# Kernel tuning notes

Hardware: AMD Instinct MI355X
Metric: run time of the kernel (lower is better)

## Reference

```python
import jax, jax.numpy as jnp
import numpy as np

NEG_SLOPE = 0.05

def setup_inputs() -> dict:
    key = jax.random.key(0)
    k1, k2, k3, k4 = jax.random.split(key, 4)
    N, C, n, l = 100000, 128, 50000, 32
    z = jax.random.normal(k1, (N, C), dtype=jnp.float32)
    # indices into table of N+1 rows (row 0 is the zero_holder pad row)
    neighbor = jax.random.randint(k2, (n, l), 0, N + 1, dtype=jnp.int64)
    w1 = jax.random.normal(k3, (C // 2, C), dtype=jnp.float32) * (1.0 / np.sqrt(C))
    w2 = jax.random.normal(k4, (C - C // 2, C // 2), dtype=jnp.float32) * (1.0 / np.sqrt(C // 2))
    return {"z": z, "neighbor": neighbor, "w1": w1, "w2": w2}

def reference(z, neighbor, w1, w2):
    # prepend zero_holder row; z is detached in the original module
    z_ = jnp.concatenate([jnp.zeros((1, z.shape[1]), dtype=z.dtype), z], axis=0)
    z_ = jax.lax.stop_gradient(z_)
    x = z_[neighbor]                       # [n, l, C] embedding gather
    # conv1d(kernel_size=1, bias=False) == per-position linear
    h1 = jnp.einsum('nlc,oc->nlo', x, w1)  # [n, l, C/2]
    h1 = jnp.where(h1 > 0, h1, NEG_SLOPE * h1)
    # dropout is identity in eval mode
    h2 = jnp.einsum('nlc,oc->nlo', h1, w2)  # [n, l, C - C/2]
    h2 = jnp.where(h2 > 0, h2, NEG_SLOPE * h2)
    cat = jnp.concatenate([h1, h2], axis=-1)  # [n, l, C]
    return jnp.max(cat, axis=1)               # adaptive_max_pool1d over l -> [n, C]
```

## Files before the change

### kernel.cpp

```cpp
#include <hip/hip_runtime.h>
#include <hip/hip_bf16.h>

typedef __attribute__((ext_vector_type(8))) short bf16x8;
typedef __attribute__((ext_vector_type(4))) short s16x4;
typedef __attribute__((ext_vector_type(4))) float f32x4;

__device__ __forceinline__ short f2bf(float f) {
    __hip_bfloat16 h = __float2bfloat16(f);
    short s;
    __builtin_memcpy(&s, &h, 2);
    return s;
}

__device__ __forceinline__ float bf2f(short s) {
    const unsigned u = (unsigned)(unsigned short)s;
    return __uint_as_float(u << 16);
}

__device__ __forceinline__ float lrelu(float v) {
    return fmaxf(v, 0.05f * v);
}

#define MFMA(a, b, c) __builtin_amdgcn_mfma_f32_16x16x32_bf16((a), (b), (c), 0, 0, 0)

__global__ __launch_bounds__(256) void mlp_rows_q8_kernel(
    const float* __restrict__ z,
    const float* __restrict__ w1,
    const float* __restrict__ w2,
    char* __restrict__ q8,
    float* __restrict__ scales,
    int rows_p1)
{
    __shared__ __align__(16) short wlds[12288];

    const int tid = threadIdx.x;
    const int lane = tid & 63;
    const int g = lane >> 4;
    const int u = lane & 15;

    #pragma unroll
    for (int j = 0; j < 12; ++j) {
        const int c = tid + (j << 8);
        const float* src;
        int row, col, fbase;
        if (c < 2048) {
            row = c >> 5; col = (c & 31) << 2;
            src = w1 + row * 128 + col;
            fbase = ((row >> 4) << 2) + (col >> 5);
        } else {
            const int c2 = c - 2048;
            row = c2 >> 4; col = (c2 & 15) << 2;
            src = w2 + row * 64 + col;
            fbase = 16 + ((row >> 4) << 1) + (col >> 5);
        }
        const int rem = col & 31;
        const int gg = (rem >> 2) & 3;
        const int eh = rem >> 4;
        float4 v = *reinterpret_cast<const float4*>(src);
        s16x4 p;
        p[0] = f2bf(v.x); p[1] = f2bf(v.y); p[2] = f2bf(v.z); p[3] = f2bf(v.w);
        const int idx = ((fbase << 6) + (gg << 4) + (row & 15)) * 8 + (eh << 2);
        *reinterpret_cast<s16x4*>(&wlds[idx]) = p;
    }
    __syncthreads();

    const bf16x8* __restrict__ wv = reinterpret_cast<const bf16x8*>(wlds);

    const int waves_per_blk = blockDim.x >> 6;
    const int wave = blockIdx.x * waves_per_blk + (tid >> 6);
    const int nwaves = gridDim.x * waves_per_blk;
    const int ntiles = (rows_p1 + 15) >> 4;

    for (int c = wave; c < ntiles; c += nwaves) {
        const int r = (c << 4) + u;
        const bool valid = (r >= 1) && (r < rows_p1);
        const bool st = r < rows_p1;

        bf16x8 bx[4];
        {
            const float* srcp = z + (size_t)(r - 1) * 128 + 4 * g;
            #pragma unroll
            for (int s = 0; s < 4; ++s) {
                float4 lo = make_float4(0.f, 0.f, 0.f, 0.f);
                float4 hi = make_float4(0.f, 0.f, 0.f, 0.f);
                if (valid) {
                    lo = *reinterpret_cast<const float4*>(srcp + 32 * s);
                    hi = *reinterpret_cast<const float4*>(srcp + 32 * s + 16);
                }
                bf16x8 f;
                f[0] = f2bf(lo.x); f[1] = f2bf(lo.y); f[2] = f2bf(lo.z); f[3] = f2bf(lo.w);
                f[4] = f2bf(hi.x); f[5] = f2bf(hi.y); f[6] = f2bf(hi.z); f[7] = f2bf(hi.w);
                bx[s] = f;
            }
        }

        char* qp = q8 + (size_t)r * 128 + 4 * g;

        f32x4 d2[4];
        #pragma unroll
        for (int b2 = 0; b2 < 4; ++b2)
            d2[b2] = (f32x4){0.f, 0.f, 0.f, 0.f};

        bf16x8 h1sav[2];

        #pragma unroll
        for (int s2 = 0; s2 < 2; ++s2) {
            bf16x8 p2;
            #pragma unroll
            for (int h = 0; h < 2; ++h) {
                const int b = 2 * s2 + h;
                f32x4 d1 = (f32x4){0.f, 0.f, 0.f, 0.f};
                #pragma unroll
                for (int s = 0; s < 4; ++s)
                    d1 = MFMA(wv[((b << 2) + s) * 64 + lane], bx[s], d1);
                #pragma unroll
                for (int q = 0; q < 4; ++q)
                    p2[4 * h + q] = f2bf(lrelu(d1[q]));
            }
            h1sav[s2] = p2;
            #pragma unroll
            for (int b2 = 0; b2 < 4; ++b2)
                d2[b2] = MFMA(wv[1024 + ((b2 << 1) + s2) * 64 + lane], p2, d2[b2]);
        }

        {
            float s1 = 0.f;
            #pragma unroll
            for (int s2 = 0; s2 < 2; ++s2)
                #pragma unroll
                for (int i = 0; i < 8; ++i)
                    s1 = fmaxf(s1, fabsf(bf2f(h1sav[s2][i])));
            s1 = fmaxf(s1, __shfl_xor(s1, 16, 64));
            s1 = fmaxf(s1, __shfl_xor(s1, 32, 64));
            const float inv = (s1 > 0.f) ? 127.f / s1 : 0.f;
            if (g == 0 && st) scales[2 * r + 0] = s1 * (1.f / 127.f);
            #pragma unroll
            for (int b = 0; b < 4; ++b) {
                unsigned pk = 0;
                #pragma unroll
                for (int q = 0; q < 4; ++q) {
                    const float hv = bf2f(h1sav[b >> 1][4 * (b & 1) + q]);
                    const int qi = __float2int_rn(hv * inv);
                    pk |= ((unsigned)(qi & 0xff)) << (8 * q);
                }
                if (st) *reinterpret_cast<unsigned*>(qp + 16 * b) = pk;
            }
        }

        {
            float s2m = 0.f;
            #pragma unroll
            for (int b2 = 0; b2 < 4; ++b2)
                #pragma unroll
                for (int q = 0; q < 4; ++q)
                    s2m = fmaxf(s2m, fabsf(lrelu(d2[b2][q])));
            s2m = fmaxf(s2m, __shfl_xor(s2m, 16, 64));
            s2m = fmaxf(s2m, __shfl_xor(s2m, 32, 64));
            const float inv = (s2m > 0.f) ? 127.f / s2m : 0.f;
            if (g == 0 && st) scales[2 * r + 1] = s2m * (1.f / 127.f);
            #pragma unroll
            for (int b2 = 0; b2 < 4; ++b2) {
                unsigned pk = 0;
                #pragma unroll
                for (int q = 0; q < 4; ++q) {
                    const int qi = __float2int_rn(lrelu(d2[b2][q]) * inv);
                    pk |= ((unsigned)(qi & 0xff)) << (8 * q);
                }
                if (st) *reinterpret_cast<unsigned*>(qp + 64 + 16 * b2) = pk;
            }
        }
    }
}

__global__ __launch_bounds__(256) void gather_max_q8_kernel(
    const char* __restrict__ q8,
    const float* __restrict__ scales,
    const int* __restrict__ neigh,
    float* __restrict__ out,
    int n_rows)
{
    const int tid = threadIdx.x;
    const int lane = tid & 63;
    const int hsel = lane >> 5;
    const int waves_per_blk = blockDim.x >> 6;
    const int wave0 = blockIdx.x * waves_per_blk + (tid >> 6);
    const int nwaves = gridDim.x * waves_per_blk;

    for (int n = wave0; n < n_rows; n += nwaves) {
        const int idxv = neigh[(size_t)n * 32 + (lane & 31)];
        const float sv = scales[(size_t)2 * (unsigned)idxv + hsel];

        unsigned short d[32];
        #pragma unroll
        for (int p = 0; p < 32; ++p) {
            const unsigned rp = (unsigned)__builtin_amdgcn_readlane(idxv, p);
            d[p] = *reinterpret_cast<const unsigned short*>(
                q8 + (size_t)rp * 128 + 2 * lane);
        }

        float m0 = -3.4e38f, m1 = -3.4e38f;
        #pragma unroll
        for (int p = 0; p < 32; ++p) {
            const float sc = __shfl(sv, (lane & 32) + p, 64);
            const int q0 = (int)(signed char)(d[p] & 0xff);
            const int q1 = (int)(signed char)(d[p] >> 8);
            m0 = fmaxf(m0, (float)q0 * sc);
            m1 = fmaxf(m1, (float)q1 * sc);
        }

        *reinterpret_cast<float2*>(out + (size_t)n * 128 + 2 * lane) =
            make_float2(m0, m1);
    }
}

struct WaveCtx {
    const bf16x8* wv;
    const int* neigh;
    float* out;
    int lane, g, u, n_rows;
};

__device__ __forceinline__ void compute_n(const WaveCtx& cx, bf16x8 (&bx)[2][4], int n)
{
    f32x4 d2[4][2];
    #pragma unroll
    for (int b2 = 0; b2 < 4; ++b2) {
        d2[b2][0] = (f32x4){0.f, 0.f, 0.f, 0.f};
        d2[b2][1] = (f32x4){0.f, 0.f, 0.f, 0.f};
    }
    float V1[16], V2[16];

    #pragma unroll
    for (int s2 = 0; s2 < 2; ++s2) {
        bf16x8 p2[2];
        #pragma unroll
        for (int h = 0; h < 2; ++h) {
            const int b = 2 * s2 + h;
            f32x4 d1[2];
            d1[0] = (f32x4){0.f, 0.f, 0.f, 0.f};
            d1[1] = (f32x4){0.f, 0.f, 0.f, 0.f};
            #pragma unroll
            for (int s = 0; s < 4; ++s) {
                const bf16x8 wf = cx.wv[((b << 2) + s) * 64 + cx.lane];
                d1[0] = MFMA(wf, bx[0][s], d1[0]);
                d1[1] = MFMA(wf, bx[1][s], d1[1]);
            }
            #pragma unroll
            for (int t = 0; t < 2; ++t) {
                #pragma unroll
                for (int q = 0; q < 4; ++q) {
                    float v = lrelu(d1[t][q]);
                    d1[t][q] = v;
                    p2[t][4 * h + q] = f2bf(v);
                }
            }
            #pragma unroll
            for (int q = 0; q < 4; ++q)
                V1[b * 4 + q] = fmaxf(d1[0][q], d1[1][q]);
        }
        #pragma unroll
        for (int b2 = 0; b2 < 4; ++b2) {
            const bf16x8 wf = cx.wv[1024 + ((b2 << 1) + s2) * 64 + cx.lane];
            d2[b2][0] = MFMA(wf, p2[0], d2[b2][0]);
            d2[b2][1] = MFMA(wf, p2[1], d2[b2][1]);
        }
    }

    #pragma unroll
    for (int b2 = 0; b2 < 4; ++b2) {
        #pragma unroll
        for (int q = 0; q < 4; ++q)
            V2[b2 * 4 + q] = lrelu(fmaxf(d2[b2][0][q], d2[b2][1][q]));
    }

    const int u = cx.u;
    #pragma unroll
    for (int k = 0; k < 4; ++k) {
        const int m = 1 << k;
        const bool hi = (u & m) != 0;
        #pragma unroll
        for (int j = 0; j < (8 >> k); ++j) {
            float k1 = hi ? V1[2 * j + 1] : V1[2 * j];
            float s1 = hi ? V1[2 * j] : V1[2 * j + 1];
            float k2 = hi ? V2[2 * j + 1] : V2[2 * j];
            float s2v = hi ? V2[2 * j] : V2[2 * j + 1];
            V1[j] = fmaxf(k1, __shfl_xor(s1, m, 64));
            V2[j] = fmaxf(k2, __shfl_xor(s2v, m, 64));
        }
    }

    const int l = cx.lane;
    const int src = 16 * ((l >> 2) & 3) + ((l >> 4) << 2) + (l & 3);
    float v1 = __shfl(V1[0], src, 64);
    float v2 = __shfl(V2[0], src, 64);
    float* op = cx.out + (size_t)n * 128;
    op[l] = v1;
    op[64 + l] = v2;
}

__global__ __launch_bounds__(256, 3) void neigh_enco_fp32_kernel(
    const float* __restrict__ z,
    const int* __restrict__ neigh,
    const float* __restrict__ w1,
    const float* __restrict__ w2,
    float* __restrict__ out,
    int n_rows, int z_rows)
{
    __shared__ __align__(16) short wlds[12288];
    const int tid = threadIdx.x;
    const int lane = tid & 63;
    const int g = lane >> 4;
    const int u = lane & 15;

    #pragma unroll
    for (int j = 0; j < 12; ++j) {
        const int c = tid + (j << 8);
        const float* src;
        int row, col, fbase;
        if (c < 2048) {
            row = c >> 5; col = (c & 31) << 2;
            src = w1 + row * 128 + col;
            fbase = ((row >> 4) << 2) + (col >> 5);
        } else {
            const int c2 = c - 2048;
            row = c2 >> 4; col = (c2 & 15) << 2;
            src = w2 + row * 64 + col;
            fbase = 16 + ((row >> 4) << 1) + (col >> 5);
        }
        const int rem = col & 31;
        const int gg = (rem >> 2) & 3;
        const int eh = rem >> 4;
        float4 v = *reinterpret_cast<const float4*>(src);
        s16x4 p;
        p[0] = f2bf(v.x); p[1] = f2bf(v.y); p[2] = f2bf(v.z); p[3] = f2bf(v.w);
        const int idx = ((fbase << 6) + (gg << 4) + (row & 15)) * 8 + (eh << 2);
        *reinterpret_cast<s16x4*>(&wlds[idx]) = p;
    }
    __syncthreads();

    WaveCtx cx;
    cx.wv = reinterpret_cast<const bf16x8*>(wlds);
    cx.neigh = neigh; cx.out = out;
    cx.lane = lane; cx.g = g; cx.u = u; cx.n_rows = n_rows;

    const int waves_per_blk = blockDim.x >> 6;
    const int wave = blockIdx.x * waves_per_blk + (tid >> 6);
    const int nwaves = gridDim.x * waves_per_blk;
    const unsigned zu = (unsigned)z_rows;

    for (int n = wave; n < n_rows; n += nwaves) {
        unsigned r0 = (unsigned)neigh[n * 32 + u] - 1u;
        unsigned r1 = (unsigned)neigh[n * 32 + 16 + u] - 1u;
        bf16x8 bx[2][4];
        #pragma unroll
        for (int t = 0; t < 2; ++t) {
            const unsigned r = t ? r1 : r0;
            const bool valid = r < zu;
            const float* base = z + (size_t)r * 128 + 4 * g;
            #pragma unroll
            for (int s = 0; s < 4; ++s) {
                float4 lo = make_float4(0.f, 0.f, 0.f, 0.f);
                float4 hi = make_float4(0.f, 0.f, 0.f, 0.f);
                if (valid) {
                    lo = *reinterpret_cast<const float4*>(base + 32 * s);
                    hi = *reinterpret_cast<const float4*>(base + 32 * s + 16);
                }
                bf16x8 f;
                f[0] = f2bf(lo.x); f[1] = f2bf(lo.y); f[2] = f2bf(lo.z); f[3] = f2bf(lo.w);
                f[4] = f2bf(hi.x); f[5] = f2bf(hi.y); f[6] = f2bf(hi.z); f[7] = f2bf(hi.w);
                bx[t][s] = f;
            }
        }
        compute_n(cx, bx, n);
    }
}

extern "C" void kernel_launch(void* const* d_in, const int* in_sizes, int n_in,
                              void* d_out, int out_size, void* d_ws, size_t ws_size,
                              hipStream_t stream) {
    const float* z     = (const float*)d_in[0];
    const int*   neigh = (const int*)d_in[1];
    const float* w1    = (const float*)d_in[2];
    const float* w2    = (const float*)d_in[3];
    float* out = (float*)d_out;
    const int z_rows = in_sizes[0] / 128;
    const int n_rows = in_sizes[1] / 32;
    const int rows_p1 = z_rows + 1;

    const size_t q8_bytes = (size_t)rows_p1 * 128;
    const size_t need = q8_bytes + (size_t)rows_p1 * 2 * sizeof(float);
    if (ws_size >= need) {
        char* q8 = (char*)d_ws;
        float* scales = (float*)((char*)d_ws + q8_bytes);
        const int ntiles = (rows_p1 + 15) / 16;
        const int blocks = (ntiles + 3) / 4;
        hipLaunchKernelGGL(mlp_rows_q8_kernel, dim3(blocks), dim3(256),
                           0, stream, z, w1, w2, q8, scales, rows_p1);
        hipLaunchKernelGGL(gather_max_q8_kernel, dim3(2048), dim3(256), 0, stream,
                           q8, scales, neigh, out, n_rows);
    } else {
        hipLaunchKernelGGL(neigh_enco_fp32_kernel, dim3(2048), dim3(256), 0, stream,
                           z, neigh, w1, w2, out, n_rows, z_rows);
    }
}
```

Baseline: 59.17 us.

## Stage z tiles through swizzled LDS and load gather scales per neighbor

The MLP kernel now cooperatively loads a 64-row chunk of z into LDS with coalesced float4 reads, converting to bf16 once and XOR-swizzling to avoid bank conflicts. Each wave then reads its MFMA operands from LDS instead of issuing strided global loads. The gather kernel drops the cross-lane shuffle for scales and instead loads both scales per neighbor row as a float2, processing neighbors in two halves of 16 to lower register pressure, and its grid is doubled. The per-chunk syncs add barrier overhead, and the extra LDS lowers occupancy in the MLP kernel.

After: 64.34 us. 1.09x slower.

```diff
diff --git a/kernel.cpp b/kernel.cpp
--- a/kernel.cpp
+++ b/kernel.cpp
@@ -32,6 +32,7 @@
     int rows_p1)
 {
     __shared__ __align__(16) short wlds[12288];
+    __shared__ __align__(16) short zlds[8192];
 
     const int tid = threadIdx.x;
     const int lane = tid & 63;
@@ -62,34 +63,46 @@
         const int idx = ((fbase << 6) + (gg << 4) + (row & 15)) * 8 + (eh << 2);
         *reinterpret_cast<s16x4*>(&wlds[idx]) = p;
     }
-    __syncthreads();
 
     const bf16x8* __restrict__ wv = reinterpret_cast<const bf16x8*>(wlds);
-
-    const int waves_per_blk = blockDim.x >> 6;
-    const int wave = blockIdx.x * waves_per_blk + (tid >> 6);
-    const int nwaves = gridDim.x * waves_per_blk;
-    const int ntiles = (rows_p1 + 15) >> 4;
-
-    for (int c = wave; c < ntiles; c += nwaves) {
-        const int r = (c << 4) + u;
-        const bool valid = (r >= 1) && (r < rows_p1);
+    const int w = tid >> 6;
+    const int nchunks = (rows_p1 + 63) >> 6;
+
+    for (int c = blockIdx.x; c < nchunks; c += gridDim.x) {
+        const int base = c << 6;
+
+        #pragma unroll
+        for (int j = 0; j < 8; ++j) {
+            const int ch = tid + (j << 8);
+            const int r = ch >> 5;
+            const int cq = (ch & 31) << 2;
+            const int gr = base + r;
+            float4 v = make_float4(0.f, 0.f, 0.f, 0.f);
+            if (gr >= 1 && gr < rows_p1)
+                v = *reinterpret_cast<const float4*>(z + (size_t)(gr - 1) * 128 + cq);
+            s16x4 p;
+            p[0] = f2bf(v.x); p[1] = f2bf(v.y); p[2] = f2bf(v.z); p[3] = f2bf(v.w);
+            const int bo = (cq << 1) ^ ((r & 7) << 4);
+            *reinterpret_cast<s16x4*>(reinterpret_cast<char*>(zlds) + r * 256 + bo) = p;
+        }
+        __syncthreads();
+
+        const int rl = 16 * w + u;
+        const int r = base + rl;
         const bool st = r < rows_p1;
 
         bf16x8 bx[4];
         {
-            const float* srcp = z + (size_t)(r - 1) * 128 + 4 * g;
+            const char* zrow = reinterpret_cast<const char*>(zlds) + rl * 256;
+            const int sw = (rl & 7) << 4;
             #pragma unroll
             for (int s = 0; s < 4; ++s) {
-                float4 lo = make_float4(0.f, 0.f, 0.f, 0.f);
-                float4 hi = make_float4(0.f, 0.f, 0.f, 0.f);
-                if (valid) {
-                    lo = *reinterpret_cast<const float4*>(srcp + 32 * s);
-                    hi = *reinterpret_cast<const float4*>(srcp + 32 * s + 16);
-                }
+                const int bo = 64 * s + 8 * g;
+                s16x4 lo = *reinterpret_cast<const s16x4*>(zrow + (bo ^ sw));
+                s16x4 hi = *reinterpret_cast<const s16x4*>(zrow + ((bo + 32) ^ sw));
                 bf16x8 f;
-                f[0] = f2bf(lo.x); f[1] = f2bf(lo.y); f[2] = f2bf(lo.z); f[3] = f2bf(lo.w);
-                f[4] = f2bf(hi.x); f[5] = f2bf(hi.y); f[6] = f2bf(hi.z); f[7] = f2bf(hi.w);
+                f[0] = lo[0]; f[1] = lo[1]; f[2] = lo[2]; f[3] = lo[3];
+                f[4] = hi[0]; f[5] = hi[1]; f[6] = hi[2]; f[7] = hi[3];
                 bx[s] = f;
             }
         }
@@ -169,6 +182,7 @@
                 if (st) *reinterpret_cast<unsigned*>(qp + 64 + 16 * b2) = pk;
             }
         }
+        __syncthreads();
     }
 }
 
@@ -181,31 +195,37 @@
 {
     const int tid = threadIdx.x;
     const int lane = tid & 63;
-    const int hsel = lane >> 5;
+    const bool hsel = (lane & 32) != 0;
     const int waves_per_blk = blockDim.x >> 6;
     const int wave0 = blockIdx.x * waves_per_blk + (tid >> 6);
     const int nwaves = gridDim.x * waves_per_blk;
 
     for (int n = wave0; n < n_rows; n += nwaves) {
         const int idxv = neigh[(size_t)n * 32 + (lane & 31)];
-        const float sv = scales[(size_t)2 * (unsigned)idxv + hsel];
-
-        unsigned short d[32];
-        #pragma unroll
-        for (int p = 0; p < 32; ++p) {
-            const unsigned rp = (unsigned)__builtin_amdgcn_readlane(idxv, p);
-            d[p] = *reinterpret_cast<const unsigned short*>(
-                q8 + (size_t)rp * 128 + 2 * lane);
-        }
 
         float m0 = -3.4e38f, m1 = -3.4e38f;
         #pragma unroll
-        for (int p = 0; p < 32; ++p) {
-            const float sc = __shfl(sv, (lane & 32) + p, 64);
-            const int q0 = (int)(signed char)(d[p] & 0xff);
-            const int q1 = (int)(signed char)(d[p] >> 8);
-            m0 = fmaxf(m0, (float)q0 * sc);
-            m1 = fmaxf(m1, (float)q1 * sc);
+        for (int half = 0; half < 2; ++half) {
+            unsigned short d[16];
+            float sA[16], sB[16];
+            #pragma unroll
+            for (int p = 0; p < 16; ++p) {
+                const int rp = __builtin_amdgcn_readlane(idxv, half * 16 + p);
+                d[p] = *reinterpret_cast<const unsigned short*>(
+                    q8 + (size_t)(unsigned)rp * 128 + 2 * lane);
+                const float2 s2 = *reinterpret_cast<const float2*>(
+                    scales + 2 * (size_t)(unsigned)rp);
+                sA[p] = s2.x;
+                sB[p] = s2.y;
+            }
+            #pragma unroll
+            for (int p = 0; p < 16; ++p) {
+                const float sc = hsel ? sB[p] : sA[p];
+                const int q0 = (int)(signed char)(d[p] & 0xff);
+                const int q1 = (int)(signed char)(d[p] >> 8);
+                m0 = fmaxf(m0, (float)q0 * sc);
+                m1 = fmaxf(m1, (float)q1 * sc);
+            }
         }
 
         *reinterpret_cast<float2*>(out + (size_t)n * 128 + 2 * lane) =
@@ -392,11 +412,10 @@
     if (ws_size >= need) {
         char* q8 = (char*)d_ws;
         float* scales = (float*)((char*)d_ws + q8_bytes);
-        const int ntiles = (rows_p1 + 15) / 16;
-        const int blocks = (ntiles + 3) / 4;
-        hipLaunchKernelGGL(mlp_rows_q8_kernel, dim3(blocks), dim3(256),
+        const int nchunks64 = (rows_p1 + 63) / 64;
+        hipLaunchKernelGGL(mlp_rows_q8_kernel, dim3(nchunks64), dim3(256),
                            0, stream, z, w1, w2, q8, scales, rows_p1);
-        hipLaunchKernelGGL(gather_max_q8_kernel, dim3(2048), dim3(256), 0, stream,
+        hipLaunchKernelGGL(gather_max_q8_kernel, dim3(4096), dim3(256), 0, stream,
                            q8, scales, neigh, out, n_rows);
     } else {
         hipLaunchKernelGGL(neigh_enco_fp32_kernel, dim3(2048), dim3(256), 0, stream,
```

## Requantize rows to global int8 scales so gather max works in integers

Applied to the files above, without the earlier changes.

The MLP kernel now also reduces global per-half max magnitudes via atomics. A new requant pass rescales every int8 row to shared global scales, so the gather kernel can take integer max without per-neighbor scale loads and shuffles. The gather kernel also processes two output rows per wave for more memory-level parallelism. This adds an extra pass over the q8 table and a memset, and double rounding loses precision for rows with small magnitude.

Measured after the change: 194.6 us. 229% more time.

```diff
diff --git a/kernel.cpp b/kernel.cpp
--- a/kernel.cpp
+++ b/kernel.cpp
@@ -28,7 +28,8 @@
     const float* __restrict__ w1,
     const float* __restrict__ w2,
     char* __restrict__ q8,
-    float* __restrict__ scales,
+    float* __restrict__ rowscales,
+    unsigned* __restrict__ gmax,
     int rows_p1)
 {
     __shared__ __align__(16) short wlds[12288];
@@ -71,6 +72,8 @@
     const int nwaves = gridDim.x * waves_per_blk;
     const int ntiles = (rows_p1 + 15) >> 4;
 
+    float wm1 = 0.f, wm2 = 0.f;
+
     for (int c = wave; c < ntiles; c += nwaves) {
         const int r = (c << 4) + u;
         const bool valid = (r >= 1) && (r < rows_p1);
@@ -132,8 +135,9 @@
                     s1 = fmaxf(s1, fabsf(bf2f(h1sav[s2][i])));
             s1 = fmaxf(s1, __shfl_xor(s1, 16, 64));
             s1 = fmaxf(s1, __shfl_xor(s1, 32, 64));
+            wm1 = fmaxf(wm1, s1);
             const float inv = (s1 > 0.f) ? 127.f / s1 : 0.f;
-            if (g == 0 && st) scales[2 * r + 0] = s1 * (1.f / 127.f);
+            if (g == 0 && st) rowscales[2 * r + 0] = s1 * (1.f / 127.f);
             #pragma unroll
             for (int b = 0; b < 4; ++b) {
                 unsigned pk = 0;
@@ -156,8 +160,9 @@
                     s2m = fmaxf(s2m, fabsf(lrelu(d2[b2][q])));
             s2m = fmaxf(s2m, __shfl_xor(s2m, 16, 64));
             s2m = fmaxf(s2m, __shfl_xor(s2m, 32, 64));
+            wm2 = fmaxf(wm2, s2m);
             const float inv = (s2m > 0.f) ? 127.f / s2m : 0.f;
-            if (g == 0 && st) scales[2 * r + 1] = s2m * (1.f / 127.f);
+            if (g == 0 && st) rowscales[2 * r + 1] = s2m * (1.f / 127.f);
             #pragma unroll
             for (int b2 = 0; b2 < 4; ++b2) {
                 unsigned pk = 0;
@@ -170,46 +175,93 @@
             }
         }
     }
-}
-
-__global__ __launch_bounds__(256) void gather_max_q8_kernel(
+
+    #pragma unroll
+    for (int m = 1; m <= 32; m <<= 1) {
+        wm1 = fmaxf(wm1, __shfl_xor(wm1, m, 64));
+        wm2 = fmaxf(wm2, __shfl_xor(wm2, m, 64));
+    }
+    if (lane == 0) {
+        atomicMax(gmax + 0, __float_as_uint(wm1));
+        atomicMax(gmax + 1, __float_as_uint(wm2));
+    }
+}
+
+__global__ __launch_bounds__(256) void requant_kernel(
+    char* __restrict__ q8,
+    const float* __restrict__ rowscales,
+    const unsigned* __restrict__ gmax,
+    int rows_p1)
+{
+    const float g1 = __uint_as_float(gmax[0]);
+    const float g2 = __uint_as_float(gmax[1]);
+    const float inv1 = (g1 > 0.f) ? 127.f / g1 : 0.f;
+    const float inv2 = (g2 > 0.f) ? 127.f / g2 : 0.f;
+    const int total = rows_p1 * 32;
+    const int stride = gridDim.x * blockDim.x;
+    for (int i = blockIdx.x * blockDim.x + threadIdx.x; i < total; i += stride) {
+        const int r = i >> 5;
+        const int c4 = i & 31;
+        const bool h2 = c4 >= 16;
+        const float f = rowscales[2 * r + (h2 ? 1 : 0)] * (h2 ? inv2 : inv1);
+        unsigned v = *reinterpret_cast<const unsigned*>(q8 + (size_t)i * 4);
+        unsigned o = 0;
+        #pragma unroll
+        for (int b = 0; b < 4; ++b) {
+            const int q = (int)(signed char)((v >> (8 * b)) & 0xff);
+            const int qn = __float2int_rn((float)q * f);
+            o |= ((unsigned)(qn & 0xff)) << (8 * b);
+        }
+        *reinterpret_cast<unsigned*>(q8 + (size_t)i * 4) = o;
+    }
+}
+
+__global__ __launch_bounds__(256) void gather_max_i8_kernel(
     const char* __restrict__ q8,
-    const float* __restrict__ scales,
+    const unsigned* __restrict__ gmax,
     const int* __restrict__ neigh,
     float* __restrict__ out,
     int n_rows)
 {
     const int tid = threadIdx.x;
     const int lane = tid & 63;
-    const int hsel = lane >> 5;
-    const int waves_per_blk = blockDim.x >> 6;
-    const int wave0 = blockIdx.x * waves_per_blk + (tid >> 6);
-    const int nwaves = gridDim.x * waves_per_blk;
-
-    for (int n = wave0; n < n_rows; n += nwaves) {
-        const int idxv = neigh[(size_t)n * 32 + (lane & 31)];
-        const float sv = scales[(size_t)2 * (unsigned)idxv + hsel];
-
-        unsigned short d[32];
+    const float sc = __uint_as_float(gmax[(lane >> 5) & 1]) * (1.f / 127.f);
+    const int wpb = blockDim.x >> 6;
+    const int wave0 = blockIdx.x * wpb + (tid >> 6);
+    const int nwaves = gridDim.x * wpb;
+    const int npairs = (n_rows + 1) >> 1;
+
+    for (int pr = wave0; pr < npairs; pr += nwaves) {
+        const int n0 = 2 * pr;
+        const int n1 = (n0 + 1 < n_rows) ? n0 + 1 : n0;
+        const int iv0 = neigh[(size_t)n0 * 32 + (lane & 31)];
+        const int iv1 = neigh[(size_t)n1 * 32 + (lane & 31)];
+
+        unsigned short d0[32], d1[32];
         #pragma unroll
         for (int p = 0; p < 32; ++p) {
-            const unsigned rp = (unsigned)__builtin_amdgcn_readlane(idxv, p);
-            d[p] = *reinterpret_cast<const unsigned short*>(
-                q8 + (size_t)rp * 128 + 2 * lane);
-        }
-
-        float m0 = -3.4e38f, m1 = -3.4e38f;
+            const unsigned r0 = (unsigned)__builtin_amdgcn_readlane(iv0, p);
+            const unsigned r1 = (unsigned)__builtin_amdgcn_readlane(iv1, p);
+            d0[p] = *reinterpret_cast<const unsigned short*>(
+                q8 + (size_t)r0 * 128 + 2 * lane);
+            d1[p] = *reinterpret_cast<const unsigned short*>(
+                q8 + (size_t)r1 * 128 + 2 * lane);
+        }
+
+        int a0 = -128, a1 = -128, b0 = -128, b1 = -128;
         #pragma unroll
         for (int p = 0; p < 32; ++p) {
-            const float sc = __shfl(sv, (lane & 32) + p, 64);
-            const int q0 = (int)(signed char)(d[p] & 0xff);
-            const int q1 = (int)(signed char)(d[p] >> 8);
-            m0 = fmaxf(m0, (float)q0 * sc);
-            m1 = fmaxf(m1, (float)q1 * sc);
-        }
-
-        *reinterpret_cast<float2*>(out + (size_t)n * 128 + 2 * lane) =
-            make_float2(m0, m1);
+            a0 = max(a0, (int)(signed char)(d0[p] & 0xff));
+            a1 = max(a1, (int)(signed char)(d0[p] >> 8));
+            b0 = max(b0, (int)(signed char)(d1[p] & 0xff));
+            b1 = max(b1, (int)(signed char)(d1[p] >> 8));
+        }
+
+        *reinterpret_cast<float2*>(out + (size_t)n0 * 128 + 2 * lane) =
+            make_float2((float)a0 * sc, (float)a1 * sc);
+        if (n1 != n0)
+            *reinterpret_cast<float2*>(out + (size_t)n1 * 128 + 2 * lane) =
+                make_float2((float)b0 * sc, (float)b1 * sc);
     }
 }
 
@@ -387,17 +439,26 @@
     const int n_rows = in_sizes[1] / 32;
     const int rows_p1 = z_rows + 1;
 
+    const size_t q8_off = 256;
     const size_t q8_bytes = (size_t)rows_p1 * 128;
-    const size_t need = q8_bytes + (size_t)rows_p1 * 2 * sizeof(float);
+    const size_t sc_off = q8_off + q8_bytes;
+    const size_t need = sc_off + (size_t)rows_p1 * 2 * sizeof(float);
+
     if (ws_size >= need) {
-        char* q8 = (char*)d_ws;
-        float* scales = (float*)((char*)d_ws + q8_bytes);
+        unsigned* gmax = (unsigned*)d_ws;
+        char* q8 = (char*)d_ws + q8_off;
+        float* rowscales = (float*)((char*)d_ws + sc_off);
+
+        hipMemsetAsync(d_ws, 0, 256, stream);
+
         const int ntiles = (rows_p1 + 15) / 16;
         const int blocks = (ntiles + 3) / 4;
         hipLaunchKernelGGL(mlp_rows_q8_kernel, dim3(blocks), dim3(256),
-                           0, stream, z, w1, w2, q8, scales, rows_p1);
-        hipLaunchKernelGGL(gather_max_q8_kernel, dim3(2048), dim3(256), 0, stream,
-                           q8, scales, neigh, out, n_rows);
+                           0, stream, z, w1, w2, q8, rowscales, gmax, rows_p1);
+        hipLaunchKernelGGL(requant_kernel, dim3(2048), dim3(256),
+                           0, stream, q8, rowscales, (const unsigned*)gmax, rows_p1);
+        hipLaunchKernelGGL(gather_max_i8_kernel, dim3(4096), dim3(256),
+                           0, stream, q8, (const unsigned*)gmax, neigh, out, n_rows);
     } else {
         hipLaunchKernelGGL(neigh_enco_fp32_kernel, dim3(2048), dim3(256), 0, stream,
                            z, neigh, w1, w2, out, n_rows, z_rows);
```

## Stage z tiles and q8 output through LDS for coalesced loads and stores

Applied to the files above, without the earlier changes.

The MLP kernel now loads each 16-row z tile with fully coalesced float4 loads, converts it to bf16 into a per-wave LDS buffer, and reads the MFMA operands back from LDS. The per-lane 4-byte scattered q8 stores are replaced by a swizzled LDS staging area followed by 16-byte coalesced row stores. The gather kernel now reads neighbor indices as wave-uniform scalar loads instead of using readlane from a vector load. This adds LDS traffic and a larger LDS footprint per block, which may cut occupancy, in exchange for better global memory access patterns.

Result: slower. 63.95 us (+8.1%).

```diff
diff --git a/kernel.cpp b/kernel.cpp
--- a/kernel.cpp
+++ b/kernel.cpp
@@ -32,11 +32,13 @@
     int rows_p1)
 {
     __shared__ __align__(16) short wlds[12288];
+    __shared__ __align__(16) char zst[4][4224];
 
     const int tid = threadIdx.x;
     const int lane = tid & 63;
     const int g = lane >> 4;
     const int u = lane & 15;
+    const int w = tid >> 6;
 
     #pragma unroll
     for (int j = 0; j < 12; ++j) {
@@ -65,36 +67,45 @@
     __syncthreads();
 
     const bf16x8* __restrict__ wv = reinterpret_cast<const bf16x8*>(wlds);
-
-    const int waves_per_blk = blockDim.x >> 6;
-    const int wave = blockIdx.x * waves_per_blk + (tid >> 6);
-    const int nwaves = gridDim.x * waves_per_blk;
+    char* const zw = zst[w];
+
+    const int wave = blockIdx.x * 4 + w;
+    const int nwaves = gridDim.x * 4;
     const int ntiles = (rows_p1 + 15) >> 4;
 
     for (int c = wave; c < ntiles; c += nwaves) {
-        const int r = (c << 4) + u;
-        const bool valid = (r >= 1) && (r < rows_p1);
+        const int base = c << 4;
+
+        {
+            const int rl = lane >> 5;
+            const int col = (lane & 31) << 2;
+            #pragma unroll
+            for (int j = 0; j < 8; ++j) {
+                const int row = 2 * j + rl;
+                const int gr = base + row;
+                float4 v = make_float4(0.f, 0.f, 0.f, 0.f);
+                if (gr >= 1 && gr < rows_p1)
+                    v = *reinterpret_cast<const float4*>(
+                        z + (size_t)(gr - 1) * 128 + col);
+                s16x4 p;
+                p[0] = f2bf(v.x); p[1] = f2bf(v.y); p[2] = f2bf(v.z); p[3] = f2bf(v.w);
+                *reinterpret_cast<s16x4*>(zw + row * 264 + col * 2) = p;
+            }
+        }
+
+        bf16x8 bx[4];
+        #pragma unroll
+        for (int s = 0; s < 4; ++s) {
+            s16x4 lo = *reinterpret_cast<const s16x4*>(zw + u * 264 + 64 * s + 8 * g);
+            s16x4 hi = *reinterpret_cast<const s16x4*>(zw + u * 264 + 64 * s + 32 + 8 * g);
+            bf16x8 f;
+            f[0] = lo[0]; f[1] = lo[1]; f[2] = lo[2]; f[3] = lo[3];
+            f[4] = hi[0]; f[5] = hi[1]; f[6] = hi[2]; f[7] = hi[3];
+            bx[s] = f;
+        }
+
+        const int r = base + u;
         const bool st = r < rows_p1;
-
-        bf16x8 bx[4];
-        {
-            const float* srcp = z + (size_t)(r - 1) * 128 + 4 * g;
-            #pragma unroll
-            for (int s = 0; s < 4; ++s) {
-                float4 lo = make_float4(0.f, 0.f, 0.f, 0.f);
-                float4 hi = make_float4(0.f, 0.f, 0.f, 0.f);
-                if (valid) {
-                    lo = *reinterpret_cast<const float4*>(srcp + 32 * s);
-                    hi = *reinterpret_cast<const float4*>(srcp + 32 * s + 16);
-                }
-                bf16x8 f;
-                f[0] = f2bf(lo.x); f[1] = f2bf(lo.y); f[2] = f2bf(lo.z); f[3] = f2bf(lo.w);
-                f[4] = f2bf(hi.x); f[5] = f2bf(hi.y); f[6] = f2bf(hi.z); f[7] = f2bf(hi.w);
-                bx[s] = f;
-            }
-        }
-
-        char* qp = q8 + (size_t)r * 128 + 4 * g;
 
         f32x4 d2[4];
         #pragma unroll
@@ -122,6 +133,8 @@
             for (int b2 = 0; b2 < 4; ++b2)
                 d2[b2] = MFMA(wv[1024 + ((b2 << 1) + s2) * 64 + lane], p2, d2[b2]);
         }
+
+        const int swz = (u & 7) << 4;
 
         {
             float s1 = 0.f;
@@ -143,7 +156,8 @@
                     const int qi = __float2int_rn(hv * inv);
                     pk |= ((unsigned)(qi & 0xff)) << (8 * q);
                 }
-                if (st) *reinterpret_cast<unsigned*>(qp + 16 * b) = pk;
+                *reinterpret_cast<unsigned*>(
+                    zw + u * 144 + (((16 * b) ^ swz) + 4 * g)) = pk;
             }
         }
 
@@ -166,7 +180,20 @@
                     const int qi = __float2int_rn(lrelu(d2[b2][q]) * inv);
                     pk |= ((unsigned)(qi & 0xff)) << (8 * q);
                 }
-                if (st) *reinterpret_cast<unsigned*>(qp + 64 + 16 * b2) = pk;
+                *reinterpret_cast<unsigned*>(
+                    zw + u * 144 + (((64 + 16 * b2) ^ swz) + 4 * g)) = pk;
+            }
+        }
+
+        #pragma unroll
+        for (int i = 0; i < 2; ++i) {
+            const int row = 8 * i + (lane >> 3);
+            const int c16 = (lane & 7) * 16;
+            if (base + row < rows_p1) {
+                uint4 v = *reinterpret_cast<const uint4*>(
+                    zw + row * 144 + (c16 ^ ((row & 7) << 4)));
+                *reinterpret_cast<uint4*>(
+                    q8 + (size_t)(base + row) * 128 + c16) = v;
             }
         }
     }
@@ -187,13 +214,16 @@
     const int nwaves = gridDim.x * waves_per_blk;
 
     for (int n = wave0; n < n_rows; n += nwaves) {
-        const int idxv = neigh[(size_t)n * 32 + (lane & 31)];
-        const float sv = scales[(size_t)2 * (unsigned)idxv + hsel];
+        const int nu = __builtin_amdgcn_readfirstlane(n);
+        const int* __restrict__ np = neigh + (size_t)nu * 32;
+
+        const int idxv = np[lane & 31];
+        const float sv = scales[2 * (size_t)(unsigned)idxv + hsel];
 
         unsigned short d[32];
         #pragma unroll
         for (int p = 0; p < 32; ++p) {
-            const unsigned rp = (unsigned)__builtin_amdgcn_readlane(idxv, p);
+            const unsigned rp = (unsigned)np[p];
             d[p] = *reinterpret_cast<const unsigned short*>(
                 q8 + (size_t)rp * 128 + 2 * lane);
         }
```
